# Kernel optimization log

Measured on AMD Instinct MI355X. Metric: run time of the kernel, lower is better.

## Reference

```python
import jax, jax.numpy as jnp
import numpy as np

EMB = 768
BLOCK = 64
K = EMB // BLOCK  # 12


def setup_inputs() -> dict:
    key = jax.random.key(0)
    ks = jax.random.split(key, 8)
    n, c, d, h, E, M, P = 4, 1024, 768, 12, 32, 4, 256
    seq = jax.random.normal(ks[0], (n, c, d), dtype=jnp.float32)
    attn = jax.random.uniform(ks[1], (n, h, c, c), dtype=jnp.float32)
    attn = attn / attn.sum(-1, keepdims=True)  # attention-like rows
    mention_pos = jax.random.randint(ks[2], (n, E, M), 0, c)
    hts = jax.random.randint(ks[3], (n, P, 2), 0, E)
    W_head = jax.random.normal(ks[4], (2 * d, EMB), dtype=jnp.float32) / np.sqrt(2 * d)
    W_tail = jax.random.normal(ks[5], (2 * d, EMB), dtype=jnp.float32) / np.sqrt(2 * d)
    W_bil = jax.random.normal(ks[6], (EMB * BLOCK, 97), dtype=jnp.float32) / np.sqrt(EMB * BLOCK)
    return {
        "sequence_output": seq,
        "attention": attn,
        "mention_pos": mention_pos,
        "hts": hts,
        "W_head": W_head,
        "b_head": jnp.zeros((EMB,), jnp.float32),
        "W_tail": W_tail,
        "b_tail": jnp.zeros((EMB,), jnp.float32),
        "W_bil": W_bil,
        "b_bil": jnp.zeros((97,), jnp.float32),
    }


def reference(sequence_output, attention, mention_pos, hts,
              W_head, b_head, W_tail, b_tail, W_bil, b_bil):
    n, c, d = sequence_output.shape
    h = attention.shape[1]
    P = hts.shape[1]

    bidx = jnp.arange(n)[:, None, None]
    # gather mention token embeddings: [n, E, M, d]
    m_emb = sequence_output[bidx, mention_pos]
    # entity embedding = logsumexp over mentions (single-mention case is identical)
    ent_emb = jax.nn.logsumexp(m_emb, axis=2)                      # [n, E, d]

    # per-mention attention rows: attention[i, :, pos, :] -> [n, E, M, h, c]
    att_t = jnp.transpose(attention, (0, 2, 1, 3))                 # [n, c, h, c]
    m_att = att_t[bidx, mention_pos]                               # [n, E, M, h, c]
    ent_att = m_att.mean(axis=2)                                   # [n, E, h, c]

    pidx = jnp.arange(n)[:, None]
    hs = ent_emb[pidx, hts[..., 0]]                                # [n, P, d]
    ts = ent_emb[pidx, hts[..., 1]]
    h_att = ent_att[pidx, hts[..., 0]]                             # [n, P, h, c]
    t_att = ent_att[pidx, hts[..., 1]]

    ht_att = (h_att * t_att).mean(axis=2)                          # [n, P, c]
    ht_att = ht_att / (ht_att.sum(-1, keepdims=True) + 1e-30)
    # relation context: contract('ld,rl->rd') per doc
    rs = jnp.einsum('ncd,npc->npd', sequence_output, ht_att)       # [n, P, d]

    R = n * P
    hs2 = jnp.tanh(jnp.concatenate([hs, rs], -1).reshape(R, 2 * d) @ W_head + b_head)
    ts2 = jnp.tanh(jnp.concatenate([ts, rs], -1).reshape(R, 2 * d) @ W_tail + b_tail)

    b1 = hs2.reshape(R, K, BLOCK)
    b2 = ts2.reshape(R, K, BLOCK)
    bl = (b1[:, :, :, None] * b2[:, :, None, :]).reshape(R, EMB * BLOCK)
    logits = bl @ W_bil + b_bil                                    # [R, 97]
    return logits
```

## Files before the change

### kernel.cpp

```cpp
#include <hip/hip_runtime.h>
#include <hip/hip_bf16.h>
#include <math.h>

#define ND 4
#define CL 1024
#define DD 768
#define HH 12
#define EE 32
#define MMEN 4
#define PP 256
#define EMBD 768
#define KBL 12
#define OUTD 97
#define RTOT (ND*PP)
#define NSPLIT 48

typedef unsigned short u16;
typedef __attribute__((ext_vector_type(8))) short short8;
typedef __attribute__((ext_vector_type(8))) _Float16 half8;
typedef __attribute__((ext_vector_type(4))) float f32x4;

static __device__ inline float bf16u_to_f(unsigned v){
  union { unsigned u; float f; } c; c.u = v << 16; return c.f;
}
static __device__ inline unsigned f_to_bf16u(float f){
  union { float f; unsigned u; } c; c.f = f;
  return (c.u + 0x7fffu + ((c.u >> 16) & 1u)) >> 16;
}
static __device__ inline u16 f_to_f16u(float f){
  _Float16 h = (_Float16)f;
  union { _Float16 h; u16 u; } c; c.h = h; return c.u;
}

#define GLOAD_LDS16(gp, lp) __builtin_amdgcn_global_load_lds( \
    (const __attribute__((address_space(1))) unsigned*)(gp), \
    (__attribute__((address_space(3))) unsigned*)(lp), 16, 0, 0)

__global__ __launch_bounds__(256) void k_preproc(
    const float* __restrict__ seq, const float* __restrict__ attn,
    const int* __restrict__ mpos,
    const float* __restrict__ W_head, const float* __restrict__ W_tail,
    const float* __restrict__ W_bil,
    u16* __restrict__ ent_emb_bf, u16* __restrict__ ent_att_bf,
    u16* __restrict__ seq_t_bf, u16* __restrict__ Wh_t, u16* __restrict__ Wt_t,
    u16* __restrict__ Wt2, float* __restrict__ S)
{
  __shared__ float t[32][33];
  __shared__ __align__(16) u16 lds2[4480];
  const int bid = blockIdx.x;
  const int tid = threadIdx.x;

  if (bid < 384) {
    int idx = bid*256 + tid;
    if (idx < RTOT) S[idx] = 0.f;
    int dd = idx % DD;
    int e  = (idx / DD) % EE;
    int i  = idx / (DD*EE);
    const int* mp = mpos + (i*EE + e)*MMEN;
    float v[MMEN];
    float mx = -1e30f;
    #pragma unroll
    for (int m=0;m<MMEN;m++){
      v[m] = seq[(i*CL + mp[m])*DD + dd];
      mx = fmaxf(mx, v[m]);
    }
    float s = 0.f;
    #pragma unroll
    for (int m=0;m<MMEN;m++) s += expf(v[m]-mx);
    ent_emb_bf[idx] = (u16)f_to_bf16u(mx + logf(s));
  }
  else if (bid < 1152) {
    int idx = (bid-384)*256 + tid;
    int j8   = idx % (CL/8);
    int head = (idx / (CL/8)) % HH;
    int e    = (idx / (CL/8*HH)) % EE;
    int i    = idx / (CL/8*HH*EE);
    const int* mp = mpos + (i*EE + e)*MMEN;
    float acc[8] = {};
    #pragma unroll
    for (int m=0;m<MMEN;m++){
      const float4* p = (const float4*)(attn +
          ((size_t)(i*HH + head)*CL + mp[m])*CL + j8*8);
      float4 a = p[0], b = p[1];
      acc[0]+=a.x; acc[1]+=a.y; acc[2]+=a.z; acc[3]+=a.w;
      acc[4]+=b.x; acc[5]+=b.y; acc[6]+=b.z; acc[7]+=b.w;
    }
    unsigned o[4];
    #pragma unroll
    for (int q=0;q<4;q++){
      unsigned lo = f_to_bf16u(acc[2*q]   * (1.f/MMEN));
      unsigned hi = f_to_bf16u(acc[2*q+1] * (1.f/MMEN));
      o[q] = lo | (hi<<16);
    }
    ((uint4*)ent_att_bf)[idx] = make_uint4(o[0],o[1],o[2],o[3]);
  }
  else if (bid < 4224) {
    int l = bid - 1152;
    int bx = l % 24;
    int by = (l / 24) % 32;
    int bz = l / 768;
    const int R = CL, C = DD;
    const float* src = seq + (size_t)bz*R*C;
    u16* dst = seq_t_bf + (size_t)bz*R*C;
    int tx = tid & 31, ty = tid >> 5;
    int c0 = bx*32, r0 = by*32;
    #pragma unroll
    for (int q=0;q<4;q++)
      t[ty+8*q][tx] = src[(size_t)(r0+ty+8*q)*C + c0+tx];
    __syncthreads();
    #pragma unroll
    for (int q=0;q<4;q++)
      dst[(size_t)(c0+ty+8*q)*R + r0+tx] = (u16)f_to_bf16u(t[tx][ty+8*q]);
  }
  else if (bid < 6528) {
    int l = bid - 4224;
    int bx = l % 24;
    int by = (l / 24) % 48;
    int bz = l / 1152;
    const int R = 1536, C = DD;
    const float* src = bz ? W_tail : W_head;
    u16* dst         = bz ? Wt_t   : Wh_t;
    int tx = tid & 31, ty = tid >> 5;
    int c0 = bx*32, r0 = by*32;
    #pragma unroll
    for (int q=0;q<4;q++)
      t[ty+8*q][tx] = src[(size_t)(r0+ty+8*q)*C + c0+tx];
    __syncthreads();
    #pragma unroll
    for (int q=0;q<4;q++)
      dst[(size_t)(c0+ty+8*q)*R + r0+tx] = (u16)f_to_bf16u(t[tx][ty+8*q]);
  }
  else {
    int cc = bid - 6528;
    for (int u=tid; u<4480; u+=256) lds2[u] = 0;
    __syncthreads();
    for (int u=tid; u<112*32; u+=256){
      int kk = u / 112, n = u % 112;
      if (n < OUTD)
        lds2[n*40 + kk] = f_to_f16u(W_bil[(size_t)(cc*32 + kk)*OUTD + n]);
    }
    __syncthreads();
    uint4* dst = (uint4*)(Wt2 + (size_t)cc*4480);
    const uint4* src = (const uint4*)lds2;
    for (int v=tid; v<560; v+=256) dst[v] = src[v];
  }
}

__global__ __launch_bounds__(256) void k_ht_att(const u16* __restrict__ ent_att_bf,
    const int* __restrict__ hts, u16* __restrict__ u_ht_bf, float* __restrict__ S)
{
  const int j0  = blockIdx.x*64;
  const int pb  = blockIdx.y*64;
  const int doc = blockIdx.z;
  const int tid = threadIdx.x;
  const int p_local = tid >> 2, quad = tid & 3;
  const int grow = doc*PP + pb + p_local;
  const int he = hts[grow*2+0], te = hts[grow*2+1];
  const u16* ha = ent_att_bf + ((size_t)(doc*EE + he)*HH)*CL;
  const u16* ta = ent_att_bf + ((size_t)(doc*EE + te)*HH)*CL;
  const int jj = j0 + quad*16;

  float acc[16] = {};
  #pragma unroll
  for (int h=0; h<HH; h++){
    const uint4* pa = (const uint4*)(ha + h*CL + jj);
    const uint4* pb4 = (const uint4*)(ta + h*CL + jj);
    uint4 a0 = pa[0], a1 = pa[1];
    uint4 b0 = pb4[0], b1 = pb4[1];
    unsigned ua[8] = {a0.x,a0.y,a0.z,a0.w,a1.x,a1.y,a1.z,a1.w};
    unsigned ub[8] = {b0.x,b0.y,b0.z,b0.w,b1.x,b1.y,b1.z,b1.w};
    #pragma unroll
    for (int q=0;q<8;q++){
      acc[2*q]   += bf16u_to_f(ua[q]&0xffffu) * bf16u_to_f(ub[q]&0xffffu);
      acc[2*q+1] += bf16u_to_f(ua[q]>>16)     * bf16u_to_f(ub[q]>>16);
    }
  }
  float sum = 0.f;
  unsigned o[8];
  #pragma unroll
  for (int q=0;q<8;q++){
    float v0 = acc[2*q]   * (1.f/HH);
    float v1 = acc[2*q+1] * (1.f/HH);
    sum += v0 + v1;
    o[q] = f_to_bf16u(v0) | (f_to_bf16u(v1)<<16);
  }
  uint4* dst = (uint4*)(u_ht_bf + (size_t)grow*CL + jj);
  dst[0] = make_uint4(o[0],o[1],o[2],o[3]);
  dst[1] = make_uint4(o[4],o[5],o[6],o[7]);
  sum += __shfl_xor(sum, 1, 64);
  sum += __shfl_xor(sum, 2, 64);
  if (quad == 0) atomicAdd(&S[grow], sum);
}

__global__ __launch_bounds__(256) void k_gemm_rs_mfma(
    const u16* __restrict__ u_ht_bf, const u16* __restrict__ seq_t_bf,
    const float* __restrict__ S, u16* __restrict__ rs_bf)
{
  const int rt = blockIdx.x, ct = blockIdx.y, doc = blockIdx.z;
  const u16* A  = u_ht_bf + (size_t)doc*PP*CL;
  const u16* Bt = seq_t_bf + (size_t)doc*DD*CL;
  const int row0 = rt*64, col0 = ct*64;
  __shared__ __align__(16) u16 As[64*64];
  __shared__ __align__(16) u16 Bs[64*64];
  const int tid = threadIdx.x, lane = tid & 63, wave = tid >> 6;
  const int m = lane & 15, j8 = lane >> 4;
  const int srow8 = lane >> 3, sc8 = lane & 7;
  f32x4 acc[4];
  #pragma unroll
  for (int b=0;b<4;b++) acc[b] = (f32x4){0.f,0.f,0.f,0.f};

  for (int k0 = 0; k0 < CL; k0 += 64){
    __syncthreads();
    #pragma unroll
    for (int ii=0; ii<2; ii++){
      int row = ii*32 + wave*8 + srow8;
      int gc = sc8 ^ (row & 7);
      const u16* gpA = A + (size_t)(row0+row)*CL + k0 + gc*8;
      GLOAD_LDS16(gpA, &As[(ii*32 + wave*8)*64]);
      const u16* gpB = Bt + (size_t)(col0+row)*CL + k0 + gc*8;
      GLOAD_LDS16(gpB, &Bs[(ii*32 + wave*8)*64]);
    }
    __syncthreads();
    #pragma unroll
    for (int h=0; h<2; h++){
      short8 af, bf[4];
      {
        int r = wave*16 + m;
        int c = (h*4 + j8) ^ (r & 7);
        af = *(const short8*)&As[r*64 + c*8];
      }
      #pragma unroll
      for (int nt=0; nt<4; nt++){
        int n = nt*16 + m;
        int c = (h*4 + j8) ^ (n & 7);
        bf[nt] = *(const short8*)&Bs[n*64 + c*8];
      }
      #pragma unroll
      for (int nt=0; nt<4; nt++)
        acc[nt] = __builtin_amdgcn_mfma_f32_16x16x32_bf16(af, bf[nt], acc[nt], 0,0,0);
    }
  }

  #pragma unroll
  for (int nt=0; nt<4; nt++){
    int colg = col0 + nt*16 + m;
    #pragma unroll
    for (int reg=0; reg<4; reg++){
      int rowg = doc*PP + row0 + wave*16 + j8*4 + reg;
      float sc = 1.f / (S[rowg] + 1e-30f);
      rs_bf[(size_t)rowg*DD + colg] = (u16)f_to_bf16u(acc[nt][reg] * sc);
    }
  }
}

__global__ __launch_bounds__(256) void k_gemm_ht_mfma(
    const u16* __restrict__ ent_emb_bf, const u16* __restrict__ rs_bf,
    const int* __restrict__ hts,
    const u16* __restrict__ Wht, const u16* __restrict__ Wtt,
    const float* __restrict__ b_head, const float* __restrict__ b_tail,
    u16* __restrict__ hs2h, u16* __restrict__ ts2h)
{
  const int rt = blockIdx.x, ct = blockIdx.y, z = blockIdx.z;
  const u16* Bt   = z ? Wtt : Wht;
  const float* bias = z ? b_tail : b_head;
  u16* C          = z ? ts2h : hs2h;
  const int row0 = rt*128, col0 = ct*64;
  __shared__ __align__(16) u16 As[128*64];
  __shared__ __align__(16) u16 Bs[64*64];
  const int tid = threadIdx.x, lane = tid & 63, wave = tid >> 6;
  const int m = lane & 15, j8 = lane >> 4;
  const int srow8 = lane >> 3, sc8 = lane & 7;

  const u16* gEnt[4]; const u16* gRs[4]; int gcA[4];
  #pragma unroll
  for (int ii=0; ii<4; ii++){
    int row  = ii*32 + wave*8 + srow8;
    int grow = row0 + row;
    int ent  = hts[grow*2 + z];
    gEnt[ii] = ent_emb_bf + ((size_t)((grow>>8)*EE + ent))*DD;
    gRs[ii]  = rs_bf + (size_t)grow*DD;
    gcA[ii]  = (sc8 ^ (row & 7)) * 8;
  }

  f32x4 acc[2][4];
  #pragma unroll
  for (int a=0;a<2;a++)
    #pragma unroll
    for (int b=0;b<4;b++) acc[a][b] = (f32x4){0.f,0.f,0.f,0.f};

  for (int k0 = 0; k0 < 1536; k0 += 64){
    __syncthreads();
    #pragma unroll
    for (int ii=0; ii<4; ii++){
      const u16* gp = (k0 < DD) ? (gEnt[ii] + k0 + gcA[ii])
                                : (gRs[ii] + (k0-DD) + gcA[ii]);
      GLOAD_LDS16(gp, &As[(ii*32 + wave*8)*64]);
    }
    #pragma unroll
    for (int ii=0; ii<2; ii++){
      int row = ii*32 + wave*8 + srow8;
      int gc = sc8 ^ (row & 7);
      const u16* gp = Bt + (size_t)(col0+row)*1536 + k0 + gc*8;
      GLOAD_LDS16(gp, &Bs[(ii*32 + wave*8)*64]);
    }
    __syncthreads();
    #pragma unroll
    for (int h=0; h<2; h++){
      short8 af[2], bf[4];
      #pragma unroll
      for (int mf=0; mf<2; mf++){
        int r = wave*32 + mf*16 + m;
        int c = (h*4 + j8) ^ (r & 7);
        af[mf] = *(const short8*)&As[r*64 + c*8];
      }
      #pragma unroll
      for (int nt=0; nt<4; nt++){
        int n = nt*16 + m;
        int c = (h*4 + j8) ^ (n & 7);
        bf[nt] = *(const short8*)&Bs[n*64 + c*8];
      }
      #pragma unroll
      for (int mf=0; mf<2; mf++)
        #pragma unroll
        for (int nt=0; nt<4; nt++)
          acc[mf][nt] = __builtin_amdgcn_mfma_f32_16x16x32_bf16(af[mf], bf[nt], acc[mf][nt], 0,0,0);
    }
  }

  #pragma unroll
  for (int mf=0; mf<2; mf++){
    #pragma unroll
    for (int nt=0; nt<4; nt++){
      int colg = col0 + nt*16 + m;
      float bv = bias[colg];
      #pragma unroll
      for (int reg=0; reg<4; reg++){
        int rowg = row0 + wave*32 + mf*16 + j8*4 + reg;
        C[(size_t)rowg*DD + colg] = f_to_f16u(tanhf(acc[mf][nt][reg] + bv));
      }
    }
  }
}

__global__ __launch_bounds__(256) void k_bilinear(
    const u16* __restrict__ hs2h, const u16* __restrict__ ts2h,
    const u16* __restrict__ Wt2, float* __restrict__ pbuf)
{
  const int rt = blockIdx.x;
  const int sp = blockIdx.y;
  const int kb = sp >> 2;
  const int i0 = (sp & 3) * 16;
  const int row0 = rt * 128;

  __shared__ __align__(16) u16 b1s[128][24];
  __shared__ __align__(16) u16 b2s[128][72];
  __shared__ __align__(16) u16 Ws[4480];

  const int tid = threadIdx.x;
  const int lane = tid & 63, wave = tid >> 6;
  const int m = lane & 15, j8 = lane >> 4;

  {
    int r = tid >> 1, half = tid & 1;
    uint4 v = *(const uint4*)&hs2h[(size_t)(row0+r)*EMBD + kb*64 + i0 + half*8];
    *(uint4*)&b1s[r][half*8] = v;
  }
  for (int u=tid; u<1024; u+=256){
    int r = u >> 3, seg = u & 7;
    uint4 v = *(const uint4*)&ts2h[(size_t)(row0+r)*EMBD + kb*64 + seg*8];
    *(uint4*)&b2s[r][seg*8] = v;
  }

  const uint4* gsrc = (const uint4*)(Wt2 + (size_t)(sp*32)*4480);
  uint4* ws4 = (uint4*)Ws;
  uint4 pf0, pf1, pf2;
  {
    pf0 = gsrc[tid];
    pf1 = gsrc[tid+256];
    if (tid < 48) pf2 = gsrc[tid+512];
  }

  f32x4 acc[2][7];
  #pragma unroll
  for (int f=0;f<2;f++)
    #pragma unroll
    for (int nt=0;nt<7;nt++) acc[f][nt] = (f32x4){0.f,0.f,0.f,0.f};

  for (int c=0; c<32; c++){
    __syncthreads();
    ws4[tid] = pf0; ws4[tid+256] = pf1; if (tid < 48) ws4[tid+512] = pf2;
    if (c+1 < 32){
      size_t b = (size_t)(c+1)*560;
      pf0 = gsrc[b+tid];
      pf1 = gsrc[b+tid+256];
      if (tid < 48) pf2 = gsrc[b+tid+512];
    }
    __syncthreads();

    const int i_rel = c >> 1;
    const int j0 = (c & 1) * 32;

    half8 bfr[7];
    #pragma unroll
    for (int nt=0;nt<7;nt++)
      bfr[nt] = *(const half8*)&Ws[(nt*16 + m)*40 + j8*8];

    #pragma unroll
    for (int f=0;f<2;f++){
      int r = wave*32 + f*16 + m;
      _Float16 s = *(const _Float16*)&b1s[r][i_rel];
      half8 sv = {s,s,s,s,s,s,s,s};
      half8 b2v = *(const half8*)&b2s[r][j0 + j8*8];
      half8 af = sv * b2v;
      #pragma unroll
      for (int nt=0;nt<7;nt++)
        acc[f][nt] = __builtin_amdgcn_mfma_f32_16x16x32_f16(af, bfr[nt], acc[f][nt], 0, 0, 0);
    }
  }

  float* dst = pbuf + ((size_t)sp*RTOT + row0)*112;
  #pragma unroll
  for (int f=0;f<2;f++){
    #pragma unroll
    for (int nt=0;nt<7;nt++){
      int col = nt*16 + m;
      #pragma unroll
      for (int reg=0;reg<4;reg++){
        int lrow = wave*32 + f*16 + j8*4 + reg;
        dst[(size_t)lrow*112 + col] = acc[f][nt][reg];
      }
    }
  }
}

__global__ __launch_bounds__(256) void k_reduce_logits(
    const float* __restrict__ pbuf, const float* __restrict__ b_bil,
    float* __restrict__ logits)
{
  int idx = blockIdx.x*256 + threadIdx.x;
  if (idx >= RTOT*112) return;
  int col = idx % 112, row = idx / 112;
  if (col >= OUTD) return;
  float s0 = 0.f, s1 = 0.f, s2 = 0.f, s3 = 0.f;
  const size_t stride = (size_t)RTOT*112;
  #pragma unroll
  for (int sp=0; sp<NSPLIT; sp+=4){
    s0 += pbuf[(sp+0)*stride + idx];
    s1 += pbuf[(sp+1)*stride + idx];
    s2 += pbuf[(sp+2)*stride + idx];
    s3 += pbuf[(sp+3)*stride + idx];
  }
  logits[(size_t)row*OUTD + col] = (s0+s1) + (s2+s3) + b_bil[col];
}

extern "C" void kernel_launch(void* const* d_in, const int* in_sizes, int n_in,
                              void* d_out, int out_size, void* d_ws, size_t ws_size,
                              hipStream_t stream)
{
  const float* seq    = (const float*)d_in[0];
  const float* attn   = (const float*)d_in[1];
  const int*   mpos   = (const int*)d_in[2];
  const int*   hts    = (const int*)d_in[3];
  const float* W_head = (const float*)d_in[4];
  const float* b_head = (const float*)d_in[5];
  const float* W_tail = (const float*)d_in[6];
  const float* b_tail = (const float*)d_in[7];
  const float* W_bil  = (const float*)d_in[8];
  const float* b_bil  = (const float*)d_in[9];
  float* logits = (float*)d_out;

  float* ws = (float*)d_ws;
  u16*   ent_emb_bf = (u16*)(ws + 0);
  float* S          = ws + 49152;
  u16*   rs_bf      = (u16*)(ws + 50176);
  u16*   hs2h       = (u16*)(ws + 443392);
  u16*   ts2h       = (u16*)(ws + 836608);
  u16*   Wh_t       = (u16*)(ws + 1229824);
  u16*   Wt_t       = (u16*)(ws + 1819648);
  u16*   ent_att_bf = (u16*)(ws + 2409472);
  u16*   u_ht_bf    = (u16*)(ws + 3195904);
  u16*   seq_t_bf   = (u16*)(ws + 3720192);
  u16*   Wt2        = (u16*)(ws + 5293056);
  float* pbuf       = ws + 8733696;

  k_preproc<<<8064, 256, 0, stream>>>(seq, attn, mpos, W_head, W_tail, W_bil,
      ent_emb_bf, ent_att_bf, seq_t_bf, Wh_t, Wt_t, Wt2, S);
  k_ht_att<<<dim3(16, 4, 4), 256, 0, stream>>>(ent_att_bf, hts, u_ht_bf, S);
  k_gemm_rs_mfma<<<dim3(4, 12, 4), 256, 0, stream>>>(u_ht_bf, seq_t_bf, S, rs_bf);
  k_gemm_ht_mfma<<<dim3(8, 12, 2), 256, 0, stream>>>(ent_emb_bf, rs_bf, hts,
      Wh_t, Wt_t, b_head, b_tail, hs2h, ts2h);
  k_bilinear<<<dim3(RTOT/128, NSPLIT), 256, 0, stream>>>(hs2h, ts2h, Wt2, pbuf);
  k_reduce_logits<<<(RTOT*112+255)/256, 256, 0, stream>>>(pbuf, b_bil, logits);
}
```

Before: 346.3 us.

## Halve bilinear K-splits and stage four weight chunks per sync

The bilinear kernel now uses 24 K-splits instead of 48, so each block covers 32 rows of the i-dimension and more of the reduction. Weights are staged four chunks at a time per barrier pair, which cuts syncs per block by a factor of four. This also halves the partial-sum buffer and the reduction work, but gives half as many blocks, more registers for prefetch and more LDS per block, which may lower occupancy. A small change also hoists the row-scale reciprocal out of the column loop in the rs GEMM epilogue.

```diff
diff --git a/kernel.cpp b/kernel.cpp
--- a/kernel.cpp
+++ b/kernel.cpp
@@ -13,7 +13,7 @@
 #define KBL 12
 #define OUTD 97
 #define RTOT (ND*PP)
-#define NSPLIT 48
+#define NSPLIT 24
 
 typedef unsigned short u16;
 typedef __attribute__((ext_vector_type(8))) short short8;
@@ -241,14 +241,19 @@
     }
   }
 
+  float sc[4];
+  #pragma unroll
+  for (int reg=0; reg<4; reg++){
+    int rowg = doc*PP + row0 + wave*16 + j8*4 + reg;
+    sc[reg] = 1.f / (S[rowg] + 1e-30f);
+  }
   #pragma unroll
   for (int nt=0; nt<4; nt++){
     int colg = col0 + nt*16 + m;
     #pragma unroll
     for (int reg=0; reg<4; reg++){
       int rowg = doc*PP + row0 + wave*16 + j8*4 + reg;
-      float sc = 1.f / (S[rowg] + 1e-30f);
-      rs_bf[(size_t)rowg*DD + colg] = (u16)f_to_bf16u(acc[nt][reg] * sc);
+      rs_bf[(size_t)rowg*DD + colg] = (u16)f_to_bf16u(acc[nt][reg] * sc[reg]);
     }
   }
 }
@@ -348,37 +353,40 @@
 {
   const int rt = blockIdx.x;
   const int sp = blockIdx.y;
-  const int kb = sp >> 2;
-  const int i0 = (sp & 3) * 16;
+  const int kb = sp >> 1;
+  const int i0 = (sp & 1) * 32;
   const int row0 = rt * 128;
 
-  __shared__ __align__(16) u16 b1s[128][24];
+  __shared__ __align__(16) u16 b1s[128][40];
   __shared__ __align__(16) u16 b2s[128][72];
-  __shared__ __align__(16) u16 Ws[4480];
+  __shared__ __align__(16) u16 Ws[4][4480];
 
   const int tid = threadIdx.x;
   const int lane = tid & 63, wave = tid >> 6;
   const int m = lane & 15, j8 = lane >> 4;
 
-  {
-    int r = tid >> 1, half = tid & 1;
-    uint4 v = *(const uint4*)&hs2h[(size_t)(row0+r)*EMBD + kb*64 + i0 + half*8];
-    *(uint4*)&b1s[r][half*8] = v;
-  }
-  for (int u=tid; u<1024; u+=256){
+  #pragma unroll
+  for (int q=0;q<2;q++){
+    int u = tid + q*256;
+    int r = u >> 2, seg = u & 3;
+    uint4 v = *(const uint4*)&hs2h[(size_t)(row0+r)*EMBD + kb*64 + i0 + seg*8];
+    *(uint4*)&b1s[r][seg*8] = v;
+  }
+  #pragma unroll
+  for (int q=0;q<4;q++){
+    int u = tid + q*256;
     int r = u >> 3, seg = u & 7;
     uint4 v = *(const uint4*)&ts2h[(size_t)(row0+r)*EMBD + kb*64 + seg*8];
     *(uint4*)&b2s[r][seg*8] = v;
   }
 
-  const uint4* gsrc = (const uint4*)(Wt2 + (size_t)(sp*32)*4480);
+  const uint4* gsrc = (const uint4*)(Wt2 + (size_t)(sp*64)*4480);
   uint4* ws4 = (uint4*)Ws;
-  uint4 pf0, pf1, pf2;
-  {
-    pf0 = gsrc[tid];
-    pf1 = gsrc[tid+256];
-    if (tid < 48) pf2 = gsrc[tid+512];
-  }
+  uint4 pf0,pf1,pf2,pf3,pf4,pf5,pf6,pf7,pf8;
+  pf0 = gsrc[tid];        pf1 = gsrc[tid+256];  pf2 = gsrc[tid+512];
+  pf3 = gsrc[tid+768];    pf4 = gsrc[tid+1024]; pf5 = gsrc[tid+1280];
+  pf6 = gsrc[tid+1536];   pf7 = gsrc[tid+1792];
+  if (tid < 192) pf8 = gsrc[tid+2048];
 
   f32x4 acc[2][7];
   #pragma unroll
@@ -386,35 +394,43 @@
     #pragma unroll
     for (int nt=0;nt<7;nt++) acc[f][nt] = (f32x4){0.f,0.f,0.f,0.f};
 
-  for (int c=0; c<32; c++){
-    __syncthreads();
-    ws4[tid] = pf0; ws4[tid+256] = pf1; if (tid < 48) ws4[tid+512] = pf2;
-    if (c+1 < 32){
-      size_t b = (size_t)(c+1)*560;
-      pf0 = gsrc[b+tid];
-      pf1 = gsrc[b+tid+256];
-      if (tid < 48) pf2 = gsrc[b+tid+512];
-    }
-    __syncthreads();
-
-    const int i_rel = c >> 1;
-    const int j0 = (c & 1) * 32;
-
-    half8 bfr[7];
-    #pragma unroll
-    for (int nt=0;nt<7;nt++)
-      bfr[nt] = *(const half8*)&Ws[(nt*16 + m)*40 + j8*8];
-
-    #pragma unroll
-    for (int f=0;f<2;f++){
-      int r = wave*32 + f*16 + m;
-      _Float16 s = *(const _Float16*)&b1s[r][i_rel];
-      half8 sv = {s,s,s,s,s,s,s,s};
-      half8 b2v = *(const half8*)&b2s[r][j0 + j8*8];
-      half8 af = sv * b2v;
+  for (int s=0; s<16; s++){
+    __syncthreads();
+    ws4[tid]      = pf0; ws4[tid+256]  = pf1; ws4[tid+512]  = pf2;
+    ws4[tid+768]  = pf3; ws4[tid+1024] = pf4; ws4[tid+1280] = pf5;
+    ws4[tid+1536] = pf6; ws4[tid+1792] = pf7;
+    if (tid < 192) ws4[tid+2048] = pf8;
+    if (s+1 < 16){
+      size_t b = (size_t)(s+1)*2240;
+      pf0 = gsrc[b+tid];      pf1 = gsrc[b+tid+256];  pf2 = gsrc[b+tid+512];
+      pf3 = gsrc[b+tid+768];  pf4 = gsrc[b+tid+1024]; pf5 = gsrc[b+tid+1280];
+      pf6 = gsrc[b+tid+1536]; pf7 = gsrc[b+tid+1792];
+      if (tid < 192) pf8 = gsrc[b+tid+2048];
+    }
+    __syncthreads();
+
+    #pragma unroll
+    for (int qq=0; qq<4; qq++){
+      const int c = s*4 + qq;
+      const int i_rel = c >> 1;
+      const int j0 = (c & 1) * 32;
+
+      half8 bfr[7];
       #pragma unroll
       for (int nt=0;nt<7;nt++)
-        acc[f][nt] = __builtin_amdgcn_mfma_f32_16x16x32_f16(af, bfr[nt], acc[f][nt], 0, 0, 0);
+        bfr[nt] = *(const half8*)&Ws[qq][(nt*16 + m)*40 + j8*8];
+
+      #pragma unroll
+      for (int f=0;f<2;f++){
+        int r = wave*32 + f*16 + m;
+        _Float16 sv1 = *(const _Float16*)&b1s[r][i_rel];
+        half8 sv = {sv1,sv1,sv1,sv1,sv1,sv1,sv1,sv1};
+        half8 b2v = *(const half8*)&b2s[r][j0 + j8*8];
+        half8 af = sv * b2v;
+        #pragma unroll
+        for (int nt=0;nt<7;nt++)
+          acc[f][nt] = __builtin_amdgcn_mfma_f32_16x16x32_f16(af, bfr[nt], acc[f][nt], 0, 0, 0);
+      }
     }
   }
 
```

Measured after the change: 347.2 us. No clear change (+0.3%).
